# Optimization experiments

Measured on AMD Instinct MI355X. Metric: run time of the kernel, lower is better.

The kernel has to match this reference:

```python
import jax, jax.numpy as jnp
import numpy as np

B, N, F = 8, 500000, 1000000


def setup_inputs() -> dict:
    key = jax.random.key(0)
    k1, k2 = jax.random.split(key)
    vert = jax.random.normal(k1, (B, N, 3), dtype=jnp.float32)
    faces = jax.random.randint(k2, (F, 3), 0, N, dtype=jnp.int64)
    return {"vert": vert, "faces": faces}


def _uniform_laplacian(vert, faces):
    # vert: [B, N, 3], faces: [F, 3]
    n = vert.shape[1]
    i, j, k = faces[:, 0], faces[:, 1], faces[:, 2]
    # 6 directed edges per face: dst accumulates its neighbors' positions (src)
    dst = jnp.concatenate([i, i, j, j, k, k])  # [6F]
    src = jnp.concatenate([j, k, i, k, i, j])  # [6F]
    deg = jax.ops.segment_sum(jnp.ones_like(dst, dtype=vert.dtype), dst, num_segments=n)  # [N]
    nbr_sum = jax.vmap(lambda v: jax.ops.segment_sum(v[src], dst, num_segments=n))(vert)  # [B,N,3]
    # lap = mean(neighbors) - v  (uniform Laplacian: D^{-1} A - I)
    return nbr_sum / jnp.maximum(deg, 1.0)[None, :, None] - vert


def reference(vert, faces):
    lap = _uniform_laplacian(vert, faces)          # [B, N, 3]
    curve = jnp.sqrt(jnp.sum(lap * lap, axis=-1))  # [B, N] (L2 norm over xyz)
    return curve
```

## Files before the change

### kernel.cpp

```cpp
#include <hip/hip_runtime.h>
#include <hip/hip_fp16.h>
#include <math.h>

#define BATCH 8
#define NBUK_MAX 512
#define BSHIFT 10
#define CAPB 6656
#define PACK_MASK 0x7FFFFull
#define EXP_T 1024
#define EXP_Q 4
#define EXP_FACES (EXP_T * EXP_Q)
#define SCAN_T 256
#define SCAN_E 8
#define SCAN_TILE (SCAN_T * SCAN_E)

union H2U { __half2 h; unsigned u; };

__device__ __forceinline__ long long pack3(int v, int a, int b) {
    return (long long)(((unsigned long long)(unsigned)v) |
                       ((unsigned long long)(unsigned)a << 19) |
                       ((unsigned long long)(unsigned)b << 38));
}

__global__ __launch_bounds__(EXP_T) void expand_kernel(
        const int* __restrict__ faces,
        int* __restrict__ cursor,
        long long* __restrict__ recbuf,
        int F) {
    __shared__ int hist[NBUK_MAX];
    __shared__ int gb[NBUK_MAX];
    int tid = threadIdx.x;
    if (tid < NBUK_MAX) hist[tid] = 0;
    __syncthreads();

    int fbase = blockIdx.x * EXP_FACES;
    int idx[EXP_Q][3];
    bool val[EXP_Q];
    #pragma unroll
    for (int q = 0; q < EXP_Q; ++q) {
        int f = fbase + q * EXP_T + tid;
        val[q] = f < F;
        if (val[q]) {
            idx[q][0] = faces[3 * f + 0];
            idx[q][1] = faces[3 * f + 1];
            idx[q][2] = faces[3 * f + 2];
        } else {
            idx[q][0] = 0; idx[q][1] = 0; idx[q][2] = 0;
        }
    }

    int rr[EXP_Q][3];
    #pragma unroll
    for (int q = 0; q < EXP_Q; ++q) {
        if (val[q]) {
            rr[q][0] = atomicAdd(&hist[idx[q][0] >> BSHIFT], 1);
            rr[q][1] = atomicAdd(&hist[idx[q][1] >> BSHIFT], 1);
            rr[q][2] = atomicAdd(&hist[idx[q][2] >> BSHIFT], 1);
        }
    }
    __syncthreads();

    if (tid < NBUK_MAX) {
        int h = hist[tid];
        gb[tid] = (h > 0) ? atomicAdd(&cursor[tid * 16], h) : 0;
    }
    __syncthreads();

    #pragma unroll
    for (int q = 0; q < EXP_Q; ++q) {
        if (val[q]) {
            int i = idx[q][0], j = idx[q][1], k = idx[q][2];
            int b0 = i >> BSHIFT, b1 = j >> BSHIFT, b2 = k >> BSHIFT;
            int p0 = gb[b0] + rr[q][0];
            int p1 = gb[b1] + rr[q][1];
            int p2 = gb[b2] + rr[q][2];
            if (p0 < CAPB) recbuf[(size_t)b0 * CAPB + p0] = pack3(i, j, k);
            if (p1 < CAPB) recbuf[(size_t)b1 * CAPB + p1] = pack3(j, i, k);
            if (p2 < CAPB) recbuf[(size_t)b2 * CAPB + p2] = pack3(k, i, j);
        }
    }
}

__global__ __launch_bounds__(1024) void repack_kernel(
        const float* __restrict__ vert,
        uint2* __restrict__ vh,
        int N) {
    int u = blockIdx.x * 1024 + threadIdx.x;
    if (u < N * BATCH) {
        int v = u >> 3;
        int b = u & 7;
        size_t src = ((size_t)b * N + v) * 3;
        H2U xy, zw;
        xy.h = __floats2half2_rn(vert[src], vert[src + 1]);
        zw.h = __floats2half2_rn(vert[src + 2], 0.0f);
        uint2 w; w.x = xy.u; w.y = zw.u;
        vh[u] = w;
    }
}

__device__ __forceinline__ void unpack_acc(uint2 r, float& ax, float& ay, float& az) {
    H2U xy, zw; xy.u = r.x; zw.u = r.y;
    float2 f0 = __half22float2(xy.h);
    float2 f1 = __half22float2(zw.h);
    ax += f0.x; ay += f0.y; az += f1.x;
}

__global__ __launch_bounds__(1024) void bucket_gather_kernel(
        const int* __restrict__ cursor,
        const long long* __restrict__ recbuf,
        const uint2* __restrict__ vh,
        float* __restrict__ out, int N) {
    __shared__ int cntL[1024];
    __shared__ int offL[1024];
    __shared__ int2 colbuf[CAPB];
    int tid = threadIdx.x;
    int bid = blockIdx.x;
    int v0 = bid << BSHIFT;

    int rc = cursor[bid * 16];
    int rcnt = rc < CAPB ? rc : CAPB;

    cntL[tid] = 0;
    __syncthreads();
    const long long* recs = recbuf + (size_t)bid * CAPB;
    for (int x = tid; x < rcnt; x += 1024) {
        int v = (int)((unsigned long long)recs[x] & PACK_MASK);
        atomicAdd(&cntL[v & 1023], 2);
    }
    __syncthreads();

    int myc = cntL[tid];
    for (int d = 1; d < 1024; d <<= 1) {
        int t = (tid >= d) ? cntL[tid - d] : 0;
        __syncthreads();
        cntL[tid] += t;
        __syncthreads();
    }
    int myoff = cntL[tid] - myc;
    cntL[tid] = myoff;
    offL[tid] = myoff;
    __syncthreads();

    for (int x = tid; x < rcnt; x += 1024) {
        unsigned long long r = (unsigned long long)recs[x];
        int v = (int)(r & PACK_MASK);
        int a = (int)((r >> 19) & PACK_MASK);
        int b = (int)((r >> 38) & PACK_MASK);
        int p = atomicAdd(&cntL[v & 1023], 2);
        colbuf[p >> 1] = make_int2(a, b);
    }
    __syncthreads();

    int b = tid & 7;
    for (int it = 0; it < (1 << BSHIFT) / 128; ++it) {
        int lv = (tid >> 3) + 128 * it;
        int v = v0 + lv;
        if (v >= N) continue;
        int start = offL[lv];
        int end = cntL[lv];
        int c = end - start;
        int e = start >> 1, e1 = end >> 1;

        float ax = 0.f, ay = 0.f, az = 0.f;
        for (; e + 4 <= e1; e += 4) {
            int2 s01 = colbuf[e];
            int2 s23 = colbuf[e + 1];
            int2 s45 = colbuf[e + 2];
            int2 s67 = colbuf[e + 3];
            uint2 r0 = vh[((size_t)s01.x << 3) + b];
            uint2 r1 = vh[((size_t)s01.y << 3) + b];
            uint2 r2 = vh[((size_t)s23.x << 3) + b];
            uint2 r3 = vh[((size_t)s23.y << 3) + b];
            uint2 r4 = vh[((size_t)s45.x << 3) + b];
            uint2 r5 = vh[((size_t)s45.y << 3) + b];
            uint2 r6 = vh[((size_t)s67.x << 3) + b];
            uint2 r7 = vh[((size_t)s67.y << 3) + b];
            unpack_acc(r0, ax, ay, az); unpack_acc(r1, ax, ay, az);
            unpack_acc(r2, ax, ay, az); unpack_acc(r3, ax, ay, az);
            unpack_acc(r4, ax, ay, az); unpack_acc(r5, ax, ay, az);
            unpack_acc(r6, ax, ay, az); unpack_acc(r7, ax, ay, az);
        }
        for (; e < e1; ++e) {
            int2 ss = colbuf[e];
            uint2 r0 = vh[((size_t)ss.x << 3) + b];
            uint2 r1 = vh[((size_t)ss.y << 3) + b];
            unpack_acc(r0, ax, ay, az);
            unpack_acc(r1, ax, ay, az);
        }

        float invd = 1.0f / fmaxf((float)c, 1.0f);
        float sx = 0.f, sy = 0.f, sz = 0.f;
        unpack_acc(vh[((size_t)v << 3) + b], sx, sy, sz);
        float l0 = ax * invd - sx;
        float l1 = ay * invd - sy;
        float l2 = az * invd - sz;
        out[(size_t)b * N + v] = sqrtf(l0 * l0 + l1 * l1 + l2 * l2);
    }
}


__global__ void count_only_kernel(const int* __restrict__ faces, int* __restrict__ cnt,
                                  int* __restrict__ rank, int F) {
    int f = blockIdx.x * blockDim.x + threadIdx.x;
    if (f >= F) return;
    rank[3 * f + 0] = atomicAdd(&cnt[faces[3 * f + 0]], 2);
    rank[3 * f + 1] = atomicAdd(&cnt[faces[3 * f + 1]], 2);
    rank[3 * f + 2] = atomicAdd(&cnt[faces[3 * f + 2]], 2);
}

__global__ void scan_sums_kernel(const int* __restrict__ cnt, int* __restrict__ bsums, int N) {
    __shared__ int sh[SCAN_T];
    int base = blockIdx.x * SCAN_TILE + threadIdx.x * SCAN_E;
    int s = 0;
    #pragma unroll
    for (int e = 0; e < SCAN_E; ++e)
        if (base + e < N) s += cnt[base + e];
    sh[threadIdx.x] = s;
    __syncthreads();
    for (int d = SCAN_T / 2; d > 0; d >>= 1) {
        if (threadIdx.x < (unsigned)d) sh[threadIdx.x] += sh[threadIdx.x + d];
        __syncthreads();
    }
    if (threadIdx.x == 0) bsums[blockIdx.x] = sh[0];
}

__global__ void scan_apply_kernel(const int* __restrict__ cnt, int* __restrict__ off,
                                  const int* __restrict__ bsums, int N, int nb) {
    __shared__ int shb[SCAN_T];
    __shared__ int sh[SCAN_T];
    int bv = ((int)threadIdx.x < nb) ? bsums[threadIdx.x] : 0;
    shb[threadIdx.x] = bv;
    __syncthreads();
    for (int d = 1; d < SCAN_T; d <<= 1) {
        int t = (threadIdx.x >= (unsigned)d) ? shb[threadIdx.x - d] : 0;
        __syncthreads();
        shb[threadIdx.x] += t;
        __syncthreads();
    }
    int block_prefix = (blockIdx.x > 0) ? shb[blockIdx.x - 1] : 0;

    int base = blockIdx.x * SCAN_TILE + threadIdx.x * SCAN_E;
    int vals[SCAN_E];
    int s = 0;
    #pragma unroll
    for (int e = 0; e < SCAN_E; ++e) {
        int v = (base + e < N) ? cnt[base + e] : 0;
        vals[e] = v; s += v;
    }
    sh[threadIdx.x] = s;
    __syncthreads();
    for (int d = 1; d < SCAN_T; d <<= 1) {
        int t = (threadIdx.x >= (unsigned)d) ? sh[threadIdx.x - d] : 0;
        __syncthreads();
        sh[threadIdx.x] += t;
        __syncthreads();
    }
    int excl = block_prefix + ((threadIdx.x > 0) ? sh[threadIdx.x - 1] : 0);
    #pragma unroll
    for (int e = 0; e < SCAN_E; ++e) {
        if (base + e < N) off[base + e] = excl;
        excl += vals[e];
    }
}

__global__ void fill_kernel(const int* __restrict__ faces, const int* __restrict__ off,
                            const int* __restrict__ rank, int* __restrict__ col, int F) {
    int f = blockIdx.x * blockDim.x + threadIdx.x;
    if (f >= F) return;
    int i = faces[3 * f + 0];
    int j = faces[3 * f + 1];
    int k = faces[3 * f + 2];
    int2* c2 = (int2*)col;
    c2[(off[i] + rank[3 * f + 0]) >> 1] = make_int2(j, k);
    c2[(off[j] + rank[3 * f + 1]) >> 1] = make_int2(i, k);
    c2[(off[k] + rank[3 * f + 2]) >> 1] = make_int2(i, j);
}

__global__ void gather_scalar_kernel(const float* __restrict__ vert,
                                     const int* __restrict__ cnt,
                                     const int* __restrict__ off,
                                     const int* __restrict__ col,
                                     float* __restrict__ out, int N) {
    int v = blockIdx.x * blockDim.x + threadIdx.x;
    if (v >= N) return;
    int c = cnt[v];
    int start = off[v];
    int end = start + c;
    float ax[BATCH], ay[BATCH], az[BATCH];
    #pragma unroll
    for (int b = 0; b < BATCH; ++b) { ax[b] = 0.f; ay[b] = 0.f; az[b] = 0.f; }
    for (int e = start; e < end; ++e) {
        int s = col[e];
        #pragma unroll
        for (int b = 0; b < BATCH; ++b) {
            size_t base = ((size_t)b * N + s) * 3;
            ax[b] += vert[base + 0];
            ay[b] += vert[base + 1];
            az[b] += vert[base + 2];
        }
    }
    float invd = 1.0f / fmaxf((float)c, 1.0f);
    #pragma unroll
    for (int b = 0; b < BATCH; ++b) {
        size_t base = ((size_t)b * N + v) * 3;
        float l0 = ax[b] * invd - vert[base + 0];
        float l1 = ay[b] * invd - vert[base + 1];
        float l2 = az[b] * invd - vert[base + 2];
        out[(size_t)b * N + v] = sqrtf(l0 * l0 + l1 * l1 + l2 * l2);
    }
}


static inline size_t align256(size_t x) { return (x + 255) & ~(size_t)255; }

extern "C" void kernel_launch(void* const* d_in, const int* in_sizes, int n_in,
                              void* d_out, int out_size, void* d_ws, size_t ws_size,
                              hipStream_t stream) {
    const float* vert  = (const float*)d_in[0];
    const int*   faces = (const int*)d_in[1];
    float*       out   = (float*)d_out;

    int N = out_size / BATCH;
    int F = in_sizes[1] / 3;
    int E = 6 * F;
    int NB = (N + (1 << BSHIFT) - 1) >> BSHIFT;

    char* ws = (char*)d_ws;

    size_t o_cursor = 0;
    size_t o_vh     = NBUK_MAX * 64;
    size_t o_rec    = o_vh + align256((size_t)N * BATCH * sizeof(uint2));
    size_t need     = o_rec + (size_t)NB * CAPB * 8;

    if (ws_size >= need && N <= 524288 && NB <= NBUK_MAX) {
        int*       cursor = (int*)(ws + o_cursor);
        uint2*     vh     = (uint2*)(ws + o_vh);
        long long* rec    = (long long*)(ws + o_rec);

        (void)hipMemsetAsync(cursor, 0, NBUK_MAX * 64, stream);

        int expB = (F + EXP_FACES - 1) / EXP_FACES;
        int repB = (N * BATCH + 1023) / 1024;
        expand_kernel<<<expB, EXP_T, 0, stream>>>(faces, cursor, rec, F);
        repack_kernel<<<repB, 1024, 0, stream>>>(vert, vh, N);
        bucket_gather_kernel<<<NB, 1024, 0, stream>>>(cursor, rec, vh, out, N);
        return;
    }

    int threads = 256;
    int nb = (N + SCAN_TILE - 1) / SCAN_TILE;
    size_t f_cnt   = 0;
    size_t f_off   = align256((size_t)N * 4);
    size_t f_bsums = f_off + align256((size_t)N * 4);
    size_t f_col   = f_bsums + 4096;
    size_t f_rank  = f_col + align256((size_t)E * 4);

    int* cnt   = (int*)(ws + f_cnt);
    int* off   = (int*)(ws + f_off);
    int* bsums = (int*)(ws + f_bsums);
    int* col   = (int*)(ws + f_col);
    int* rank  = (int*)(ws + f_rank);

    (void)hipMemsetAsync(cnt, 0, (size_t)N * 4, stream);

    int cntBlocks = (F + threads - 1) / threads;
    count_only_kernel<<<cntBlocks, threads, 0, stream>>>(faces, cnt, rank, F);
    scan_sums_kernel<<<nb, SCAN_T, 0, stream>>>(cnt, bsums, N);
    scan_apply_kernel<<<nb, SCAN_T, 0, stream>>>(cnt, off, bsums, N, nb);
    fill_kernel<<<cntBlocks, threads, 0, stream>>>(faces, off, rank, col, F);
    gather_scalar_kernel<<<(N + threads - 1) / threads, threads, 0, stream>>>(
        vert, cnt, off, col, out, N);
}
```

Measured before the change: 231.8 us.

## Merge expand and repack kernels; use wave-shuffle scan in bucket gather

Combines the face-expansion and vertex fp16 repack into one launch, with block ranges split by blockIdx, so the two independent stages run concurrently and one kernel launch is saved. Replaces the 10-step shared-memory Hillis-Steele scan, which had two barriers per step, with a 64-lane wavefront shuffle scan plus a 16-entry cross-wave prefix. This cuts barriers in the per-bucket offset computation. The merged kernel keeps the same register and LDS footprint for the repack blocks, which may limit their occupancy.

```diff
diff --git a/kernel.cpp b/kernel.cpp
--- a/kernel.cpp
+++ b/kernel.cpp
@@ -22,79 +22,79 @@
                        ((unsigned long long)(unsigned)b << 38));
 }
 
-__global__ __launch_bounds__(EXP_T) void expand_kernel(
+__global__ __launch_bounds__(EXP_T) void expand_repack_kernel(
         const int* __restrict__ faces,
         int* __restrict__ cursor,
         long long* __restrict__ recbuf,
-        int F) {
+        const float* __restrict__ vert,
+        uint2* __restrict__ vh,
+        int N, int F, int expBlocks) {
     __shared__ int hist[NBUK_MAX];
     __shared__ int gb[NBUK_MAX];
     int tid = threadIdx.x;
-    if (tid < NBUK_MAX) hist[tid] = 0;
-    __syncthreads();
-
-    int fbase = blockIdx.x * EXP_FACES;
-    int idx[EXP_Q][3];
-    bool val[EXP_Q];
-    #pragma unroll
-    for (int q = 0; q < EXP_Q; ++q) {
-        int f = fbase + q * EXP_T + tid;
-        val[q] = f < F;
-        if (val[q]) {
-            idx[q][0] = faces[3 * f + 0];
-            idx[q][1] = faces[3 * f + 1];
-            idx[q][2] = faces[3 * f + 2];
-        } else {
-            idx[q][0] = 0; idx[q][1] = 0; idx[q][2] = 0;
-        }
-    }
-
-    int rr[EXP_Q][3];
-    #pragma unroll
-    for (int q = 0; q < EXP_Q; ++q) {
-        if (val[q]) {
-            rr[q][0] = atomicAdd(&hist[idx[q][0] >> BSHIFT], 1);
-            rr[q][1] = atomicAdd(&hist[idx[q][1] >> BSHIFT], 1);
-            rr[q][2] = atomicAdd(&hist[idx[q][2] >> BSHIFT], 1);
-        }
-    }
-    __syncthreads();
-
-    if (tid < NBUK_MAX) {
-        int h = hist[tid];
-        gb[tid] = (h > 0) ? atomicAdd(&cursor[tid * 16], h) : 0;
-    }
-    __syncthreads();
-
-    #pragma unroll
-    for (int q = 0; q < EXP_Q; ++q) {
-        if (val[q]) {
-            int i = idx[q][0], j = idx[q][1], k = idx[q][2];
-            int b0 = i >> BSHIFT, b1 = j >> BSHIFT, b2 = k >> BSHIFT;
-            int p0 = gb[b0] + rr[q][0];
-            int p1 = gb[b1] + rr[q][1];
-            int p2 = gb[b2] + rr[q][2];
-            if (p0 < CAPB) recbuf[(size_t)b0 * CAPB + p0] = pack3(i, j, k);
-            if (p1 < CAPB) recbuf[(size_t)b1 * CAPB + p1] = pack3(j, i, k);
-            if (p2 < CAPB) recbuf[(size_t)b2 * CAPB + p2] = pack3(k, i, j);
-        }
-    }
-}
-
-__global__ __launch_bounds__(1024) void repack_kernel(
-        const float* __restrict__ vert,
-        uint2* __restrict__ vh,
-        int N) {
-    int u = blockIdx.x * 1024 + threadIdx.x;
-    if (u < N * BATCH) {
-        int v = u >> 3;
-        int b = u & 7;
-        size_t src = ((size_t)b * N + v) * 3;
-        H2U xy, zw;
-        xy.h = __floats2half2_rn(vert[src], vert[src + 1]);
-        zw.h = __floats2half2_rn(vert[src + 2], 0.0f);
-        uint2 w; w.x = xy.u; w.y = zw.u;
-        vh[u] = w;
+
+    if ((int)blockIdx.x < expBlocks) {
+        if (tid < NBUK_MAX) hist[tid] = 0;
+        __syncthreads();
+
+        int fbase = blockIdx.x * EXP_FACES;
+        int idx[EXP_Q][3];
+        bool val[EXP_Q];
+        #pragma unroll
+        for (int q = 0; q < EXP_Q; ++q) {
+            int f = fbase + q * EXP_T + tid;
+            val[q] = f < F;
+            if (val[q]) {
+                idx[q][0] = faces[3 * f + 0];
+                idx[q][1] = faces[3 * f + 1];
+                idx[q][2] = faces[3 * f + 2];
+            } else {
+                idx[q][0] = 0; idx[q][1] = 0; idx[q][2] = 0;
+            }
+        }
+
+        int rr[EXP_Q][3];
+        #pragma unroll
+        for (int q = 0; q < EXP_Q; ++q) {
+            if (val[q]) {
+                rr[q][0] = atomicAdd(&hist[idx[q][0] >> BSHIFT], 1);
+                rr[q][1] = atomicAdd(&hist[idx[q][1] >> BSHIFT], 1);
+                rr[q][2] = atomicAdd(&hist[idx[q][2] >> BSHIFT], 1);
+            }
+        }
+        __syncthreads();
+
+        if (tid < NBUK_MAX) {
+            int h = hist[tid];
+            gb[tid] = (h > 0) ? atomicAdd(&cursor[tid * 16], h) : 0;
+        }
+        __syncthreads();
+
+        #pragma unroll
+        for (int q = 0; q < EXP_Q; ++q) {
+            if (val[q]) {
+                int i = idx[q][0], j = idx[q][1], k = idx[q][2];
+                int b0 = i >> BSHIFT, b1 = j >> BSHIFT, b2 = k >> BSHIFT;
+                int p0 = gb[b0] + rr[q][0];
+                int p1 = gb[b1] + rr[q][1];
+                int p2 = gb[b2] + rr[q][2];
+                if (p0 < CAPB) recbuf[(size_t)b0 * CAPB + p0] = pack3(i, j, k);
+                if (p1 < CAPB) recbuf[(size_t)b1 * CAPB + p1] = pack3(j, i, k);
+                if (p2 < CAPB) recbuf[(size_t)b2 * CAPB + p2] = pack3(k, i, j);
+            }
+        }
+    } else {
+        int u = (blockIdx.x - expBlocks) * EXP_T + threadIdx.x;
+        if (u < N * BATCH) {
+            int v = u >> 3;
+            int b = u & 7;
+            size_t src = ((size_t)b * N + v) * 3;
+            H2U xy, zw;
+            xy.h = __floats2half2_rn(vert[src], vert[src + 1]);
+            zw.h = __floats2half2_rn(vert[src + 2], 0.0f);
+            uint2 w; w.x = xy.u; w.y = zw.u;
+            vh[u] = w;
+        }
     }
 }
 
@@ -112,6 +112,7 @@
         float* __restrict__ out, int N) {
     __shared__ int cntL[1024];
     __shared__ int offL[1024];
+    __shared__ int wsumG[16];
     __shared__ int2 colbuf[CAPB];
     int tid = threadIdx.x;
     int bid = blockIdx.x;
@@ -130,13 +131,22 @@
     __syncthreads();
 
     int myc = cntL[tid];
-    for (int d = 1; d < 1024; d <<= 1) {
-        int t = (tid >= d) ? cntL[tid - d] : 0;
-        __syncthreads();
-        cntL[tid] += t;
-        __syncthreads();
-    }
-    int myoff = cntL[tid] - myc;
+    int lane = tid & 63;
+    int wv = tid >> 6;
+    int incl = myc;
+    #pragma unroll
+    for (int d = 1; d < 64; d <<= 1) {
+        int t = __shfl_up(incl, d, 64);
+        if (lane >= d) incl += t;
+    }
+    if (lane == 63) wsumG[wv] = incl;
+    __syncthreads();
+    int pre = 0;
+    #pragma unroll
+    for (int w = 0; w < 16; ++w)
+        pre += (w < wv) ? wsumG[w] : 0;
+    incl += pre;
+    int myoff = incl - myc;
     cntL[tid] = myoff;
     offL[tid] = myoff;
     __syncthreads();
@@ -340,9 +350,10 @@
         (void)hipMemsetAsync(cursor, 0, NBUK_MAX * 64, stream);
 
         int expB = (F + EXP_FACES - 1) / EXP_FACES;
-        int repB = (N * BATCH + 1023) / 1024;
-        expand_kernel<<<expB, EXP_T, 0, stream>>>(faces, cursor, rec, F);
-        repack_kernel<<<repB, 1024, 0, stream>>>(vert, vh, N);
+        int repB = (N * BATCH + EXP_T - 1) / EXP_T;
+        expand_repack_kernel<<<expB + repB, EXP_T, 0, stream>>>(
+            faces, cursor, rec, vert, vh, N, F, expB);
+
         bucket_gather_kernel<<<NB, 1024, 0, stream>>>(cursor, rec, vh, out, N);
         return;
     }
```

New measurement: 227.6 us. Within noise of the previous version (-1.8%).
